# Optimization experiments

Hardware: AMD Instinct MI355X
Metric: run time of the kernel (lower is better)

Reference implementation:

```python
import jax, jax.numpy as jnp
import numpy as np

NUM_Q = 4        # len(n_e_list)
N_E = 2048       # codes per quantizer level
E_DIM = 128      # e_dim
N_TOK = 32768    # flattened tokens
BETA = 0.25      # commitment coefficient


def setup_inputs() -> dict:
    key = jax.random.key(0)
    k_x, k_cb = jax.random.split(key)
    x = jax.random.normal(k_x, (N_TOK, E_DIM), dtype=jnp.float32)
    codebooks = jax.random.normal(k_cb, (NUM_Q, N_E, E_DIM), dtype=jnp.float32) * 0.1
    return {"x": x, "codebooks": codebooks, "use_freq": 0}


def _vq_layer(res, cb):
    # res: [N, D], cb: [K, D]
    # squared euclidean distance via expansion: ||r||^2 - 2 r.c + ||c||^2
    d = (jnp.sum(res * res, axis=-1, keepdims=True)
         - 2.0 * (res @ cb.T)
         + jnp.sum(cb * cb, axis=-1))            # [N, K]
    idx = jnp.argmin(d, axis=-1)                  # [N]
    q = cb[idx]                                   # [N, D] gather
    sg = jax.lax.stop_gradient
    # VQ-VAE loss: codebook term + beta * commitment term
    loss = jnp.mean((q - sg(res)) ** 2) + BETA * jnp.mean((sg(q) - res) ** 2)
    q_st = res + sg(q - res)                      # straight-through estimator
    return q_st, loss, idx


def reference(x, codebooks, use_freq):
    # residual chain over NUM_Q quantizer levels (sequential dependency)
    def step(carry, cb):
        residual, x_q = carry
        q, loss, idx = _vq_layer(residual, cb)
        return (residual - q, x_q + q), (loss, idx)

    (residual, x_q), (losses, indices) = jax.lax.scan(
        step, (x, jnp.zeros_like(x)), codebooks)
    mean_loss = jnp.mean(losses)
    all_indices = jnp.moveaxis(indices, 0, -1)    # [N, NUM_Q]
    return x_q, mean_loss, all_indices
```

## Files before the change

### kernel.cpp

```cpp
#include <hip/hip_runtime.h>

#define NTOK 32768
#define NE   2048
#define EDIM 128
#define NQ   4

#define TOKT 64
#define CHCODES 128
#define NCHUNK (NE / CHCODES)
#define CAP 16
#define MARGIN_S 0.1875f

typedef __attribute__((ext_vector_type(8))) short short8v;
typedef __attribute__((ext_vector_type(4))) float f32x4;

__device__ __forceinline__ unsigned short bf16rne(float x) {
    unsigned u = __float_as_uint(x);
    unsigned r = 0x7FFFu + ((u >> 16) & 1u);
    return (unsigned short)((u + r) >> 16);
}

__device__ __forceinline__ void gld16(const void* g, const void* l) {
    __builtin_amdgcn_global_load_lds(
        (const __attribute__((address_space(1))) unsigned int*)g,
        (__attribute__((address_space(3))) unsigned int*)l, 16, 0, 0);
}

#define MFMA_BF16 __builtin_amdgcn_mfma_f32_16x16x32_bf16

__global__ __launch_bounds__(256) void prep_kernel(
    const float* __restrict__ cb, unsigned short* __restrict__ cb16s,
    float* __restrict__ cnorm, float* __restrict__ loss_accum)
{
    const int row = blockIdx.x * 256 + threadIdx.x;
    if (row == 0) *loss_accum = 0.0f;
    const float* src = cb + (size_t)row * EDIM;
    unsigned short* dst = cb16s + (size_t)row * EDIM;
    const int swz8 = (row & 7) << 3;
    float s = 0.0f;
#pragma unroll
    for (int j = 0; j < EDIM / 4; ++j) {
        float4 v = ((const float4*)src)[j];
        s += v.x * v.x; s += v.y * v.y; s += v.z * v.z; s += v.w * v.w;
        ushort4 o;
        o.x = bf16rne(v.x); o.y = bf16rne(v.y);
        o.z = bf16rne(v.z); o.w = bf16rne(v.w);
        *(ushort4*)(dst + ((j * 4) ^ swz8)) = o;
    }
    cnorm[row] = s;
}

__global__ __launch_bounds__(256, 2) void vq_level_kernel(
    const float* __restrict__ rin,
    const float* __restrict__ cbF,
    const unsigned short* __restrict__ cbL,
    const float* __restrict__ cnorm,
    float* __restrict__ rout,
    float* __restrict__ xq,
    float* __restrict__ idx_out,
    float* __restrict__ loss_accum,
    int level, int first)
{
    __shared__ __align__(16) unsigned short Bs[2][CHCODES * EDIM];
    __shared__ float part[4 * TOKT];
    __shared__ float rns[TOKT];
    __shared__ float mdw[4][TOKT];
    __shared__ float smaxs[TOKT];
    __shared__ int   cnt[TOKT];
    __shared__ int   lst[TOKT * CAP];
    __shared__ float redb_d[4][TOKT];
    __shared__ int   redb_i[4][TOKT];
    __shared__ int   idx_s[TOKT];
    __shared__ float lsum[256];

    const int t    = threadIdx.x;
    const int tok0 = blockIdx.x * TOKT;
    const int w    = t >> 6;
    const int cl   = t & 15;
    const int lg   = (t & 63) >> 4;
    if (t < TOKT) cnt[t] = 0;

    {
        const int tok = t & 63;
        const int dg  = t >> 6;
        float s = 0.0f;
#pragma unroll
        for (int j = 0; j < 8; ++j) {
            const int d0 = dg * 32 + j * 4;
            float4 v = *(const float4*)(rin + (size_t)(tok0 + tok) * EDIM + d0);
            s += v.x * v.x; s += v.y * v.y; s += v.z * v.z; s += v.w * v.w;
        }
        part[dg * TOKT + tok] = s;
    }
    __syncthreads();
    if (t < TOKT)
        rns[t] = ((part[t] + part[TOKT + t]) + part[2 * TOKT + t])
                 + part[3 * TOKT + t];

    short8v a00, a01, a02, a03, a10, a11, a12, a13;
    short8v a20, a21, a22, a23, a30, a31, a32, a33;
#define LDA(AF, RT, KT) { \
    const float* ap = rin + (size_t)(tok0 + (RT) * 16 + cl) * EDIM \
                      + (KT) * 32 + lg * 8; \
    float4 q0 = *(const float4*)ap; float4 q1 = *(const float4*)(ap + 4); \
    AF[0] = (short)bf16rne(q0.x); AF[1] = (short)bf16rne(q0.y); \
    AF[2] = (short)bf16rne(q0.z); AF[3] = (short)bf16rne(q0.w); \
    AF[4] = (short)bf16rne(q1.x); AF[5] = (short)bf16rne(q1.y); \
    AF[6] = (short)bf16rne(q1.z); AF[7] = (short)bf16rne(q1.w); }
    LDA(a00, 0, 0) LDA(a01, 0, 1) LDA(a02, 0, 2) LDA(a03, 0, 3)
    LDA(a10, 1, 0) LDA(a11, 1, 1) LDA(a12, 1, 2) LDA(a13, 1, 3)
    LDA(a20, 2, 0) LDA(a21, 2, 1) LDA(a22, 2, 2) LDA(a23, 2, 3)
    LDA(a30, 3, 0) LDA(a31, 3, 1) LDA(a32, 3, 2) LDA(a33, 3, 3)
#undef LDA

    const int swzk = (cl & 7) << 4;
    const int inn0 = (0   + lg * 16) ^ swzk;
    const int inn1 = (64  + lg * 16) ^ swzk;
    const int inn2 = (128 + lg * 16) ^ swzk;
    const int inn3 = (192 + lg * 16) ^ swzk;

    const int tb0 = lg * 4, tb1 = 16 + lg * 4, tb2 = 32 + lg * 4, tb3 = 48 + lg * 4;

#define STAGE(DST, CH) { \
    const char* gs = (const char*)cbL + (size_t)(CH) * 32768 + t * 16; \
    char* ls = (char*)(DST) + (t & 192) * 16; \
    gld16(gs,          ls); \
    gld16(gs + 4096,   ls + 4096); \
    gld16(gs + 8192,   ls + 8192); \
    gld16(gs + 12288,  ls + 12288); \
    gld16(gs + 16384,  ls + 16384); \
    gld16(gs + 20480,  ls + 20480); \
    gld16(gs + 24576,  ls + 24576); \
    gld16(gs + 28672,  ls + 28672); }

#define CTBLK(BUFC, CH, CT, TAIL) { \
    const int code = (CH) * CHCODES + w * 32 + (CT) * 16 + cl; \
    const float cn2 = -0.5f * cnorm[code]; \
    const char* bp = (const char*)&Bs[BUFC][0] \
                     + (w * 32 + (CT) * 16 + cl) * 256; \
    f32x4 p0 = {cn2, cn2, cn2, cn2}; f32x4 p1 = p0; \
    f32x4 p2 = p0;                   f32x4 p3 = p0; \
    short8v bb; \
    bb = *(const short8v*)(bp + inn0); \
    p0 = MFMA_BF16(a00, bb, p0, 0, 0, 0); p1 = MFMA_BF16(a10, bb, p1, 0, 0, 0); \
    p2 = MFMA_BF16(a20, bb, p2, 0, 0, 0); p3 = MFMA_BF16(a30, bb, p3, 0, 0, 0); \
    bb = *(const short8v*)(bp + inn1); \
    p0 = MFMA_BF16(a01, bb, p0, 0, 0, 0); p1 = MFMA_BF16(a11, bb, p1, 0, 0, 0); \
    p2 = MFMA_BF16(a21, bb, p2, 0, 0, 0); p3 = MFMA_BF16(a31, bb, p3, 0, 0, 0); \
    bb = *(const short8v*)(bp + inn2); \
    p0 = MFMA_BF16(a02, bb, p0, 0, 0, 0); p1 = MFMA_BF16(a12, bb, p1, 0, 0, 0); \
    p2 = MFMA_BF16(a22, bb, p2, 0, 0, 0); p3 = MFMA_BF16(a32, bb, p3, 0, 0, 0); \
    bb = *(const short8v*)(bp + inn3); \
    p0 = MFMA_BF16(a03, bb, p0, 0, 0, 0); p1 = MFMA_BF16(a13, bb, p1, 0, 0, 0); \
    p2 = MFMA_BF16(a23, bb, p2, 0, 0, 0); p3 = MFMA_BF16(a33, bb, p3, 0, 0, 0); \
    TAIL }

#define T_MIN \
    md00 = fmaxf(md00, p0[0]); md01 = fmaxf(md01, p0[1]); \
    md02 = fmaxf(md02, p0[2]); md03 = fmaxf(md03, p0[3]); \
    md10 = fmaxf(md10, p1[0]); md11 = fmaxf(md11, p1[1]); \
    md12 = fmaxf(md12, p1[2]); md13 = fmaxf(md13, p1[3]); \
    md20 = fmaxf(md20, p2[0]); md21 = fmaxf(md21, p2[1]); \
    md22 = fmaxf(md22, p2[2]); md23 = fmaxf(md23, p2[3]); \
    md30 = fmaxf(md30, p3[0]); md31 = fmaxf(md31, p3[1]); \
    md32 = fmaxf(md32, p3[2]); md33 = fmaxf(md33, p3[3]);

#define PUSH1(S, TH, TOK) { if ((S) > (TH)) { \
    int pp = atomicAdd(&cnt[TOK], 1); \
    if (pp < CAP) lst[(TOK) * CAP + pp] = code; } }
#define T_PUSH \
    PUSH1(p0[0], th00, tb0 + 0) PUSH1(p0[1], th01, tb0 + 1) \
    PUSH1(p0[2], th02, tb0 + 2) PUSH1(p0[3], th03, tb0 + 3) \
    PUSH1(p1[0], th10, tb1 + 0) PUSH1(p1[1], th11, tb1 + 1) \
    PUSH1(p1[2], th12, tb1 + 2) PUSH1(p1[3], th13, tb1 + 3) \
    PUSH1(p2[0], th20, tb2 + 0) PUSH1(p2[1], th21, tb2 + 1) \
    PUSH1(p2[2], th22, tb2 + 2) PUSH1(p2[3], th23, tb2 + 3) \
    PUSH1(p3[0], th30, tb3 + 0) PUSH1(p3[1], th31, tb3 + 1) \
    PUSH1(p3[2], th32, tb3 + 2) PUSH1(p3[3], th33, tb3 + 3)

#define CH_P1(B, CH) { CTBLK(B, CH, 0, T_MIN)  CTBLK(B, CH, 1, T_MIN)  }
#define CH_P2(B, CH) { CTBLK(B, CH, 0, T_PUSH) CTBLK(B, CH, 1, T_PUSH) }

    STAGE(&Bs[0][0], 0)
    __syncthreads();

    float md00 = -3.402823466e38f, md01 = md00, md02 = md00, md03 = md00;
    float md10 = md00, md11 = md00, md12 = md00, md13 = md00;
    float md20 = md00, md21 = md00, md22 = md00, md23 = md00;
    float md30 = md00, md31 = md00, md32 = md00, md33 = md00;

    for (int c2 = 0; c2 < NCHUNK / 2; ++c2) {
        const int c = c2 * 2;
        STAGE(&Bs[1][0], c + 1)
        CH_P1(0, c)
        __syncthreads();
        if (c + 2 < NCHUNK) STAGE(&Bs[0][0], c + 2)
        CH_P1(1, c + 1)
        __syncthreads();
    }

    STAGE(&Bs[0][0], 0)

#pragma unroll
    for (int m = 1; m < 16; m <<= 1) {
        md00 = fmaxf(md00, __shfl_xor(md00, m, 64));
        md01 = fmaxf(md01, __shfl_xor(md01, m, 64));
        md02 = fmaxf(md02, __shfl_xor(md02, m, 64));
        md03 = fmaxf(md03, __shfl_xor(md03, m, 64));
        md10 = fmaxf(md10, __shfl_xor(md10, m, 64));
        md11 = fmaxf(md11, __shfl_xor(md11, m, 64));
        md12 = fmaxf(md12, __shfl_xor(md12, m, 64));
        md13 = fmaxf(md13, __shfl_xor(md13, m, 64));
        md20 = fmaxf(md20, __shfl_xor(md20, m, 64));
        md21 = fmaxf(md21, __shfl_xor(md21, m, 64));
        md22 = fmaxf(md22, __shfl_xor(md22, m, 64));
        md23 = fmaxf(md23, __shfl_xor(md23, m, 64));
        md30 = fmaxf(md30, __shfl_xor(md30, m, 64));
        md31 = fmaxf(md31, __shfl_xor(md31, m, 64));
        md32 = fmaxf(md32, __shfl_xor(md32, m, 64));
        md33 = fmaxf(md33, __shfl_xor(md33, m, 64));
    }
    if (cl == 0) {
        mdw[w][tb0 + 0] = md00; mdw[w][tb0 + 1] = md01;
        mdw[w][tb0 + 2] = md02; mdw[w][tb0 + 3] = md03;
        mdw[w][tb1 + 0] = md10; mdw[w][tb1 + 1] = md11;
        mdw[w][tb1 + 2] = md12; mdw[w][tb1 + 3] = md13;
        mdw[w][tb2 + 0] = md20; mdw[w][tb2 + 1] = md21;
        mdw[w][tb2 + 2] = md22; mdw[w][tb2 + 3] = md23;
        mdw[w][tb3 + 0] = md30; mdw[w][tb3 + 1] = md31;
        mdw[w][tb3 + 2] = md32; mdw[w][tb3 + 3] = md33;
    }
    __syncthreads();
    if (t < TOKT)
        smaxs[t] = fmaxf(fmaxf(mdw[0][t], mdw[1][t]),
                         fmaxf(mdw[2][t], mdw[3][t]));
    __syncthreads();

    const float th00 = smaxs[tb0 + 0] - MARGIN_S;
    const float th01 = smaxs[tb0 + 1] - MARGIN_S;
    const float th02 = smaxs[tb0 + 2] - MARGIN_S;
    const float th03 = smaxs[tb0 + 3] - MARGIN_S;
    const float th10 = smaxs[tb1 + 0] - MARGIN_S;
    const float th11 = smaxs[tb1 + 1] - MARGIN_S;
    const float th12 = smaxs[tb1 + 2] - MARGIN_S;
    const float th13 = smaxs[tb1 + 3] - MARGIN_S;
    const float th20 = smaxs[tb2 + 0] - MARGIN_S;
    const float th21 = smaxs[tb2 + 1] - MARGIN_S;
    const float th22 = smaxs[tb2 + 2] - MARGIN_S;
    const float th23 = smaxs[tb2 + 3] - MARGIN_S;
    const float th30 = smaxs[tb3 + 0] - MARGIN_S;
    const float th31 = smaxs[tb3 + 1] - MARGIN_S;
    const float th32 = smaxs[tb3 + 2] - MARGIN_S;
    const float th33 = smaxs[tb3 + 3] - MARGIN_S;

    for (int c2 = 0; c2 < NCHUNK / 2; ++c2) {
        const int c = c2 * 2;
        STAGE(&Bs[1][0], c + 1)
        CH_P2(0, c)
        __syncthreads();
        if (c + 2 < NCHUNK) STAGE(&Bs[0][0], c + 2)
        CH_P2(1, c + 1)
        __syncthreads();
    }

    {
        const int tok = t & 63;
        const int s   = t >> 6;
        const int n   = min(cnt[tok], CAP);
        const float rn_t = rns[tok];
        const float* rrow = rin + (size_t)(tok0 + tok) * EDIM;
        float bd = 3.402823466e38f;
        int   bi = 0x7fffffff;
        for (int i = s; i < n; i += 4) {
            const int c = lst[tok * CAP + i];
            const float* cr = cbF + (size_t)c * EDIM;
            float dot = 0.0f;
#pragma unroll
            for (int j = 0; j < 32; ++j) {
                const float4 a = *(const float4*)(rrow + j * 4);
                const float4 b = *(const float4*)(cr + j * 4);
                dot = fmaf(a.x, b.x, dot); dot = fmaf(a.y, b.y, dot);
                dot = fmaf(a.z, b.z, dot); dot = fmaf(a.w, b.w, dot);
            }
            const float dd = (rn_t - 2.0f * dot) + cnorm[c];
            if (dd < bd || (dd == bd && c < bi)) { bd = dd; bi = c; }
        }
        redb_d[s][tok] = bd;
        redb_i[s][tok] = bi;
    }
    __syncthreads();
    if (t < TOKT) {
        float bd = redb_d[0][t];
        int   bi = redb_i[0][t];
#pragma unroll
        for (int s = 1; s < 4; ++s) {
            const float dd = redb_d[s][t];
            const int   ii = redb_i[s][t];
            if (dd < bd || (dd == bd && ii < bi)) { bd = dd; bi = ii; }
        }
        idx_s[t] = bi;
        idx_out[(size_t)(tok0 + t) * NQ + level] = (float)bi;
    }
    __syncthreads();

    {
        const int tok = t >> 2;
        const int dq  = t & 3;
        const int gi  = idx_s[tok];
        const float* qrow = cbF + (size_t)gi * EDIM;
        const float* rrow = rin + (size_t)(tok0 + tok) * EDIM;
        float lp = 0.0f;
#pragma unroll
        for (int k = 0; k < 8; ++k) {
            const int d0 = k * 16 + dq * 4;
            const float4 q = *(const float4*)(qrow + d0);
            const float4 r = *(const float4*)(rrow + d0);
            float4 tq, qst, rnv;
            tq.x = q.x - r.x; tq.y = q.y - r.y; tq.z = q.z - r.z; tq.w = q.w - r.w;
            qst.x = r.x + tq.x; qst.y = r.y + tq.y;
            qst.z = r.z + tq.z; qst.w = r.w + tq.w;
            rnv.x = r.x - qst.x; rnv.y = r.y - qst.y;
            rnv.z = r.z - qst.z; rnv.w = r.w - qst.w;
            const size_t go = (size_t)(tok0 + tok) * EDIM + d0;
            *(float4*)(rout + go) = rnv;
            if (first) {
                *(float4*)(xq + go) = qst;
            } else {
                float4 o = *(const float4*)(xq + go);
                o.x += qst.x; o.y += qst.y; o.z += qst.z; o.w += qst.w;
                *(float4*)(xq + go) = o;
            }
            lp += tq.x * tq.x; lp += tq.y * tq.y;
            lp += tq.z * tq.z; lp += tq.w * tq.w;
        }
        lsum[t] = lp;
    }
    __syncthreads();
#pragma unroll
    for (int s2 = 128; s2 > 0; s2 >>= 1) {
        if (t < s2) lsum[t] += lsum[t + s2];
        __syncthreads();
    }
    if (t == 0) atomicAdd(loss_accum, lsum[0]);
}

__global__ void finalize_kernel(const float* __restrict__ loss_accum,
                                float* __restrict__ out_loss)
{
    *out_loss = *loss_accum * (1.25f / (4.0f * (float)NTOK * (float)EDIM));
}

extern "C" void kernel_launch(void* const* d_in, const int* in_sizes, int n_in,
                              void* d_out, int out_size, void* d_ws, size_t ws_size,
                              hipStream_t stream)
{
    const float* x  = (const float*)d_in[0];
    const float* cb = (const float*)d_in[1];

    float* out      = (float*)d_out;
    float* xq       = out;
    float* out_loss = out + (size_t)NTOK * EDIM;
    float* idx_out  = out + (size_t)NTOK * EDIM + 1;

    float* ws             = (float*)d_ws;
    float* cnorm          = ws;
    float* loss_accum     = ws + 8192;
    unsigned short* cb16s = (unsigned short*)(ws + 8448);
    float* r0             = ws + 8448 + (size_t)NQ * NE * EDIM / 2;

    prep_kernel<<<(NQ * NE) / 256, 256, 0, stream>>>(cb, cb16s, cnorm, loss_accum);

    for (int l = 0; l < NQ; ++l) {
        const float* rin = (l == 0) ? x : r0;
        vq_level_kernel<<<NTOK / TOKT, 256, 0, stream>>>(
            rin, cb + (size_t)l * NE * EDIM,
            cb16s + (size_t)l * NE * EDIM,
            cnorm + (size_t)l * NE,
            r0, xq, idx_out, loss_accum, l, (l == 0) ? 1 : 0);
    }
    finalize_kernel<<<1, 1, 0, stream>>>(loss_accum, out_loss);
}
```

Measured before the change: 313.7 us.

## Load codebook B fragments directly from global memory instead of LDS staging

Removes the double-buffered LDS staging of bf16 codebook chunks (global_load_lds plus barriers) and the XOR swizzle. Each wave now reads its B fragments straight from global memory (L2-resident) and owns a contiguous 512-code slice instead of a 32-code slice of every chunk. This drops LDS traffic and the per-chunk __syncthreads, at the cost of exposed global-load latency and more L2 bandwidth per block, since each wave reads a disjoint codebook range without sharing.

```diff
diff --git a/kernel.cpp b/kernel.cpp
--- a/kernel.cpp
+++ b/kernel.cpp
@@ -6,8 +6,6 @@
 #define NQ   4
 
 #define TOKT 64
-#define CHCODES 128
-#define NCHUNK (NE / CHCODES)
 #define CAP 16
 #define MARGIN_S 0.1875f
 
@@ -20,23 +18,16 @@
     return (unsigned short)((u + r) >> 16);
 }
 
-__device__ __forceinline__ void gld16(const void* g, const void* l) {
-    __builtin_amdgcn_global_load_lds(
-        (const __attribute__((address_space(1))) unsigned int*)g,
-        (__attribute__((address_space(3))) unsigned int*)l, 16, 0, 0);
-}
-
 #define MFMA_BF16 __builtin_amdgcn_mfma_f32_16x16x32_bf16
 
 __global__ __launch_bounds__(256) void prep_kernel(
-    const float* __restrict__ cb, unsigned short* __restrict__ cb16s,
+    const float* __restrict__ cb, unsigned short* __restrict__ cb16,
     float* __restrict__ cnorm, float* __restrict__ loss_accum)
 {
     const int row = blockIdx.x * 256 + threadIdx.x;
     if (row == 0) *loss_accum = 0.0f;
     const float* src = cb + (size_t)row * EDIM;
-    unsigned short* dst = cb16s + (size_t)row * EDIM;
-    const int swz8 = (row & 7) << 3;
+    unsigned short* dst = cb16 + (size_t)row * EDIM;
     float s = 0.0f;
 #pragma unroll
     for (int j = 0; j < EDIM / 4; ++j) {
@@ -45,7 +36,7 @@
         ushort4 o;
         o.x = bf16rne(v.x); o.y = bf16rne(v.y);
         o.z = bf16rne(v.z); o.w = bf16rne(v.w);
-        *(ushort4*)(dst + ((j * 4) ^ swz8)) = o;
+        *(ushort4*)(dst + j * 4) = o;
     }
     cnorm[row] = s;
 }
@@ -61,7 +52,6 @@
     float* __restrict__ loss_accum,
     int level, int first)
 {
-    __shared__ __align__(16) unsigned short Bs[2][CHCODES * EDIM];
     __shared__ float part[4 * TOKT];
     __shared__ float rns[TOKT];
     __shared__ float mdw[4][TOKT];
@@ -113,46 +103,27 @@
     LDA(a30, 3, 0) LDA(a31, 3, 1) LDA(a32, 3, 2) LDA(a33, 3, 3)
 #undef LDA
 
-    const int swzk = (cl & 7) << 4;
-    const int inn0 = (0   + lg * 16) ^ swzk;
-    const int inn1 = (64  + lg * 16) ^ swzk;
-    const int inn2 = (128 + lg * 16) ^ swzk;
-    const int inn3 = (192 + lg * 16) ^ swzk;
-
     const int tb0 = lg * 4, tb1 = 16 + lg * 4, tb2 = 32 + lg * 4, tb3 = 48 + lg * 4;
-
-#define STAGE(DST, CH) { \
-    const char* gs = (const char*)cbL + (size_t)(CH) * 32768 + t * 16; \
-    char* ls = (char*)(DST) + (t & 192) * 16; \
-    gld16(gs,          ls); \
-    gld16(gs + 4096,   ls + 4096); \
-    gld16(gs + 8192,   ls + 8192); \
-    gld16(gs + 12288,  ls + 12288); \
-    gld16(gs + 16384,  ls + 16384); \
-    gld16(gs + 20480,  ls + 20480); \
-    gld16(gs + 24576,  ls + 24576); \
-    gld16(gs + 28672,  ls + 28672); }
-
-#define CTBLK(BUFC, CH, CT, TAIL) { \
-    const int code = (CH) * CHCODES + w * 32 + (CT) * 16 + cl; \
+    const int cbase = w * 512;
+
+#define CTBLK(CT, TAIL) { \
+    const int code = cbase + (CT) * 16 + cl; \
     const float cn2 = -0.5f * cnorm[code]; \
-    const char* bp = (const char*)&Bs[BUFC][0] \
-                     + (w * 32 + (CT) * 16 + cl) * 256; \
+    const unsigned short* bp = cbL + (size_t)code * EDIM + lg * 8; \
+    short8v b0 = *(const short8v*)(bp); \
+    short8v b1 = *(const short8v*)(bp + 32); \
+    short8v b2 = *(const short8v*)(bp + 64); \
+    short8v b3 = *(const short8v*)(bp + 96); \
     f32x4 p0 = {cn2, cn2, cn2, cn2}; f32x4 p1 = p0; \
     f32x4 p2 = p0;                   f32x4 p3 = p0; \
-    short8v bb; \
-    bb = *(const short8v*)(bp + inn0); \
-    p0 = MFMA_BF16(a00, bb, p0, 0, 0, 0); p1 = MFMA_BF16(a10, bb, p1, 0, 0, 0); \
-    p2 = MFMA_BF16(a20, bb, p2, 0, 0, 0); p3 = MFMA_BF16(a30, bb, p3, 0, 0, 0); \
-    bb = *(const short8v*)(bp + inn1); \
-    p0 = MFMA_BF16(a01, bb, p0, 0, 0, 0); p1 = MFMA_BF16(a11, bb, p1, 0, 0, 0); \
-    p2 = MFMA_BF16(a21, bb, p2, 0, 0, 0); p3 = MFMA_BF16(a31, bb, p3, 0, 0, 0); \
-    bb = *(const short8v*)(bp + inn2); \
-    p0 = MFMA_BF16(a02, bb, p0, 0, 0, 0); p1 = MFMA_BF16(a12, bb, p1, 0, 0, 0); \
-    p2 = MFMA_BF16(a22, bb, p2, 0, 0, 0); p3 = MFMA_BF16(a32, bb, p3, 0, 0, 0); \
-    bb = *(const short8v*)(bp + inn3); \
-    p0 = MFMA_BF16(a03, bb, p0, 0, 0, 0); p1 = MFMA_BF16(a13, bb, p1, 0, 0, 0); \
-    p2 = MFMA_BF16(a23, bb, p2, 0, 0, 0); p3 = MFMA_BF16(a33, bb, p3, 0, 0, 0); \
+    p0 = MFMA_BF16(a00, b0, p0, 0, 0, 0); p1 = MFMA_BF16(a10, b0, p1, 0, 0, 0); \
+    p2 = MFMA_BF16(a20, b0, p2, 0, 0, 0); p3 = MFMA_BF16(a30, b0, p3, 0, 0, 0); \
+    p0 = MFMA_BF16(a01, b1, p0, 0, 0, 0); p1 = MFMA_BF16(a11, b1, p1, 0, 0, 0); \
+    p2 = MFMA_BF16(a21, b1, p2, 0, 0, 0); p3 = MFMA_BF16(a31, b1, p3, 0, 0, 0); \
+    p0 = MFMA_BF16(a02, b2, p0, 0, 0, 0); p1 = MFMA_BF16(a12, b2, p1, 0, 0, 0); \
+    p2 = MFMA_BF16(a22, b2, p2, 0, 0, 0); p3 = MFMA_BF16(a32, b2, p3, 0, 0, 0); \
+    p0 = MFMA_BF16(a03, b3, p0, 0, 0, 0); p1 = MFMA_BF16(a13, b3, p1, 0, 0, 0); \
+    p2 = MFMA_BF16(a23, b3, p2, 0, 0, 0); p3 = MFMA_BF16(a33, b3, p3, 0, 0, 0); \
     TAIL }
 
 #define T_MIN \
@@ -178,28 +149,15 @@
     PUSH1(p3[0], th30, tb3 + 0) PUSH1(p3[1], th31, tb3 + 1) \
     PUSH1(p3[2], th32, tb3 + 2) PUSH1(p3[3], th33, tb3 + 3)
 
-#define CH_P1(B, CH) { CTBLK(B, CH, 0, T_MIN)  CTBLK(B, CH, 1, T_MIN)  }
-#define CH_P2(B, CH) { CTBLK(B, CH, 0, T_PUSH) CTBLK(B, CH, 1, T_PUSH) }
-
-    STAGE(&Bs[0][0], 0)
-    __syncthreads();
-
     float md00 = -3.402823466e38f, md01 = md00, md02 = md00, md03 = md00;
     float md10 = md00, md11 = md00, md12 = md00, md13 = md00;
     float md20 = md00, md21 = md00, md22 = md00, md23 = md00;
     float md30 = md00, md31 = md00, md32 = md00, md33 = md00;
 
-    for (int c2 = 0; c2 < NCHUNK / 2; ++c2) {
-        const int c = c2 * 2;
-        STAGE(&Bs[1][0], c + 1)
-        CH_P1(0, c)
-        __syncthreads();
-        if (c + 2 < NCHUNK) STAGE(&Bs[0][0], c + 2)
-        CH_P1(1, c + 1)
-        __syncthreads();
-    }
-
-    STAGE(&Bs[0][0], 0)
+#pragma unroll 2
+    for (int ct = 0; ct < 32; ++ct) {
+        CTBLK(ct, T_MIN)
+    }
 
 #pragma unroll
     for (int m = 1; m < 16; m <<= 1) {
@@ -253,15 +211,11 @@
     const float th32 = smaxs[tb3 + 2] - MARGIN_S;
     const float th33 = smaxs[tb3 + 3] - MARGIN_S;
 
-    for (int c2 = 0; c2 < NCHUNK / 2; ++c2) {
-        const int c = c2 * 2;
-        STAGE(&Bs[1][0], c + 1)
-        CH_P2(0, c)
-        __syncthreads();
-        if (c + 2 < NCHUNK) STAGE(&Bs[0][0], c + 2)
-        CH_P2(1, c + 1)
-        __syncthreads();
-    }
+#pragma unroll 2
+    for (int ct = 0; ct < 32; ++ct) {
+        CTBLK(ct, T_PUSH)
+    }
+    __syncthreads();
 
     {
         const int tok = t & 63;
@@ -365,16 +319,16 @@
     float* ws             = (float*)d_ws;
     float* cnorm          = ws;
     float* loss_accum     = ws + 8192;
-    unsigned short* cb16s = (unsigned short*)(ws + 8448);
+    unsigned short* cb16  = (unsigned short*)(ws + 8448);
     float* r0             = ws + 8448 + (size_t)NQ * NE * EDIM / 2;
 
-    prep_kernel<<<(NQ * NE) / 256, 256, 0, stream>>>(cb, cb16s, cnorm, loss_accum);
+    prep_kernel<<<(NQ * NE) / 256, 256, 0, stream>>>(cb, cb16, cnorm, loss_accum);
 
     for (int l = 0; l < NQ; ++l) {
         const float* rin = (l == 0) ? x : r0;
         vq_level_kernel<<<NTOK / TOKT, 256, 0, stream>>>(
             rin, cb + (size_t)l * NE * EDIM,
-            cb16s + (size_t)l * NE * EDIM,
+            cb16 + (size_t)l * NE * EDIM,
             cnorm + (size_t)l * NE,
             r0, xq, idx_out, loss_accum, l, (l == 0) ? 1 : 0);
     }
```

New measurement: 378.8 us. +20.7%, slower.
